# Optimization experiments

Hardware: AMD Instinct MI355X
Metric: run time of the kernel (lower is better)

The kernel has to match this reference:

```python
import jax, jax.numpy as jnp
import numpy as np

WIN = 7
HEADS = 6
DIM = 192

def _relative_position_index(ws):
    coords = np.stack(np.meshgrid(np.arange(ws[0]), np.arange(ws[1]), indexing='ij'))  # (2, Wh, Ww)
    flat = coords.reshape(2, -1)  # (2, N)
    rel = flat[:, :, None] - flat[:, None, :]  # (2, N, N)
    rel = rel.transpose(1, 2, 0).copy()
    rel[:, :, 0] += ws[0] - 1
    rel[:, :, 1] += ws[1] - 1
    idx = rel[:, :, 0] * (2 * ws[1] - 1) + rel[:, :, 1]
    return idx.astype(np.int32)  # (N, N)

def setup_inputs() -> dict:
    key = jax.random.key(0)
    ks = jax.random.split(key, 6)
    B_, N, C = 4096, WIN * WIN, DIM
    x = jax.random.normal(ks[0], (B_, N, C), dtype=jnp.float32)
    qkv_w = jax.random.normal(ks[1], (3 * C, C), dtype=jnp.float32) * 0.02
    qkv_b = jax.random.normal(ks[2], (3 * C,), dtype=jnp.float32) * 0.02
    proj_w = jax.random.normal(ks[3], (C, C), dtype=jnp.float32) * 0.02
    proj_b = jax.random.normal(ks[4], (C,), dtype=jnp.float32) * 0.02
    bias_table = jax.random.normal(ks[5], ((2 * WIN - 1) ** 2, HEADS), dtype=jnp.float32) * 0.02
    rel_idx = jnp.asarray(_relative_position_index((WIN, WIN)))  # (N, N) int32
    return {"x": x, "qkv_w": qkv_w, "qkv_b": qkv_b, "proj_w": proj_w,
            "proj_b": proj_b, "bias_table": bias_table, "rel_idx": rel_idx}

def reference(x, qkv_w, qkv_b, proj_w, proj_b, bias_table, rel_idx):
    B_, N, C = x.shape
    H = HEADS
    Dh = C // H
    scale = Dh ** -0.5
    # qkv: (B_, N, 3C) -> (3, B_, H, N, Dh)
    qkv = (x @ qkv_w.T + qkv_b).reshape(B_, N, 3, H, Dh).transpose(2, 0, 3, 1, 4)
    q, k, v = qkv[0], qkv[1], qkv[2]
    attn = jnp.einsum('bhnd,bhmd->bhnm', q, k) * scale  # (B_, H, N, N)
    bias = bias_table[rel_idx]  # (N, N, H)
    attn = attn + bias.transpose(2, 0, 1)[None]  # (1, H, N, N) broadcast
    attn = jax.nn.softmax(attn, axis=-1)
    out = jnp.einsum('bhnm,bhmd->bhnd', attn, v)  # (B_, H, N, Dh)
    out = out.transpose(0, 2, 1, 3).reshape(B_, N, C)
    return out @ proj_w.T + proj_b
```

## Files before the change

### kernel.cpp

```cpp
#include <hip/hip_runtime.h>
#include <hip/hip_bf16.h>

#define NTOK 49
#define HEADS 6
#define DIM 192
#define DH 32

typedef short s8v __attribute__((ext_vector_type(8)));
typedef float f4v __attribute__((ext_vector_type(4)));

#define MFMA16(a, b, c) __builtin_amdgcn_mfma_f32_16x16x32_bf16((a), (b), (c), 0, 0, 0)

__device__ inline short f2bf(float f) {
    __hip_bfloat16 h = __float2bfloat16(f);
    return __builtin_bit_cast(short, h);
}

__device__ inline s8v ld_bf8(const float* __restrict__ p) {
    float4 f0 = *(const float4*)p;
    float4 f1 = *(const float4*)(p + 4);
    s8v r;
    r[0] = f2bf(f0.x); r[1] = f2bf(f0.y); r[2] = f2bf(f0.z); r[3] = f2bf(f0.w);
    r[4] = f2bf(f1.x); r[5] = f2bf(f1.y); r[6] = f2bf(f1.z); r[7] = f2bf(f1.w);
    return r;
}

__global__ void prep_kernel(const float* __restrict__ qkv_w,
                            const float* __restrict__ proj_w,
                            const float* __restrict__ bias_table,
                            const int* __restrict__ rel_idx,
                            short* __restrict__ wq, short* __restrict__ wp,
                            float* __restrict__ biasM) {
    int tid = blockIdx.x * blockDim.x + threadIdx.x;
    int stride = gridDim.x * blockDim.x;
    for (int i = tid; i < 3 * DIM * DIM; i += stride) wq[i] = f2bf(qkv_w[i]);
    for (int i = tid; i < DIM * DIM; i += stride)     wp[i] = f2bf(proj_w[i]);
    for (int i = tid; i < HEADS * NTOK * NTOK; i += stride) {
        int h = i / (NTOK * NTOK), rc = i - h * (NTOK * NTOK);
        biasM[i] = bias_table[rel_idx[rc] * HEADS + h];
    }
}

__global__ __launch_bounds__(512) void qkv_kernel(
    const float* __restrict__ x, const short* __restrict__ wq,
    const float* __restrict__ qkv_b,
    short* __restrict__ q_ws, short* __restrict__ k_ws, short* __restrict__ v_ws)
{
    __shared__ __align__(16) short xs[64 * 200];
    __shared__ __align__(16) short vbuf[192 * 72];

    const int tid = threadIdx.x, w = tid >> 6, lane = tid & 63;
    const int quad = lane >> 4, l16 = lane & 15, b = blockIdx.x;

    {
        const float4* src = (const float4*)(x + (size_t)b * NTOK * DIM);
        for (int idx = tid; idx < 2352; idx += 512) {
            int n = idx / 48, c = idx % 48;
            float4 f = src[idx];
            short* dst = &xs[n * 200 + c * 4];
            dst[0] = f2bf(f.x); dst[1] = f2bf(f.y);
            dst[2] = f2bf(f.z); dst[3] = f2bf(f.w);
        }
        int* xz = (int*)xs;
        for (int i = tid; i < 1500; i += 512) xz[4900 + i] = 0;
        for (int i = tid; i < 192 * 23; i += 512) {
            int row = i / 23, t = 49 + i % 23;
            vbuf[row * 72 + t] = 0;
        }
    }
    __syncthreads();

    for (int nt = w; nt < 36; nt += 8) {
        const short* wrow = wq + (nt * 16 + l16) * DIM + quad * 8;
        s8v bw[6];
#pragma unroll
        for (int kb = 0; kb < 6; ++kb)
            bw[kb] = *(const s8v*)(wrow + kb * 32);

        f4v acc[4];
#pragma unroll
        for (int mt = 0; mt < 4; ++mt) acc[mt] = (f4v){0.f, 0.f, 0.f, 0.f};

#pragma unroll
        for (int kb = 0; kb < 6; ++kb) {
#pragma unroll
            for (int mt = 0; mt < 4; ++mt) {
                s8v a = *(const s8v*)&xs[(mt * 16 + l16) * 200 + kb * 32 + quad * 8];
                acc[mt] = MFMA16(a, bw[kb], acc[mt]);
            }
        }

        int t = nt / 12, hh = (nt % 12) >> 1, dh16 = (nt & 1) * 16;
        float bias = qkv_b[nt * 16 + l16];
        if (t == 2) {
            short* dst = &vbuf[(hh * DH + dh16 + l16) * 72];
#pragma unroll
            for (int mt = 0; mt < 4; ++mt)
#pragma unroll
                for (int r = 0; r < 4; ++r) {
                    int row = mt * 16 + quad * 4 + r;
                    if (row < NTOK) dst[row] = f2bf(acc[mt][r] + bias);
                }
        } else {
            float scale = (t == 0) ? 0.17677669529663689f : 1.0f;
            short* dst = (t == 0 ? q_ws : k_ws)
                       + (size_t)(b * HEADS + hh) * NTOK * DH + dh16 + l16;
#pragma unroll
            for (int mt = 0; mt < 4; ++mt)
#pragma unroll
                for (int r = 0; r < 4; ++r) {
                    int row = mt * 16 + quad * 4 + r;
                    if (row < NTOK) dst[row * DH] = f2bf((acc[mt][r] + bias) * scale);
                }
        }
    }
    __syncthreads();

    {
        short* dstbase = v_ws + (size_t)b * 192 * 64;
        for (int c = tid; c < 1536; c += 512) {
            int row = c >> 3, tk = (c & 7) * 8;
            *(int4*)(dstbase + row * 64 + tk) = *(const int4*)&vbuf[row * 72 + tk];
        }
    }
}

__global__ __launch_bounds__(384) void attn_kernel(
    const short* __restrict__ k_ws, const short* __restrict__ v_ws,
    const float* __restrict__ biasM, short* qo_ws )
{
    __shared__ __align__(16) short ps[6 * 64 * 72];

    const int tid = threadIdx.x, w = tid >> 6, lane = tid & 63;
    const int quad = lane >> 4, l16 = lane & 15, b = blockIdx.x;
    const int h = w;
    short* psw = ps + w * 4608;

    const short* qb = qo_ws + (size_t)(b * HEADS + h) * NTOK * DH;
    const short* kb = k_ws  + (size_t)(b * HEADS + h) * NTOK * DH;
    const short* vb = v_ws  + (size_t)(b * HEADS + h) * DH * 64;

    s8v aq[4], bk[4];
    for (int i = 0; i < 4; ++i)
        aq[i] = *(const s8v*)(qb + (i * 16 + l16) * DH + quad * 8);
    for (int i = 0; i < 4; ++i)
        bk[i] = *(const s8v*)(kb + (i * 16 + l16) * DH + quad * 8);

    f4v sacc[4][4];
    for (int mt = 0; mt < 4; ++mt)
        for (int nt = 0; nt < 4; ++nt)
            sacc[mt][nt] = MFMA16(aq[mt], bk[nt], ((f4v){0.f, 0.f, 0.f, 0.f}));

    const float* bmh = biasM + h * (NTOK * NTOK);
    for (int mt = 0; mt < 4; ++mt)
        for (int r = 0; r < 4; ++r) {
            int row = mt * 16 + quad * 4 + r;
            float sv[4];
            for (int nt = 0; nt < 4; ++nt) {
                int col = nt * 16 + l16;
                float s = sacc[mt][nt][r];
                if (col < NTOK) {
                    if (row < NTOK) s += bmh[row * NTOK + col];
                } else s = -30000.f;
                sv[nt] = s;
            }
            float m = fmaxf(fmaxf(sv[0], sv[1]), fmaxf(sv[2], sv[3]));
            for (int d = 1; d < 16; d <<= 1) m = fmaxf(m, __shfl_xor(m, d));
            float p[4], sum = 0.f;
            for (int nt = 0; nt < 4; ++nt) {
                p[nt] = exp2f((sv[nt] - m) * 1.4426950408889634f);
                sum += p[nt];
            }
            for (int d = 1; d < 16; d <<= 1) sum += __shfl_xor(sum, d);
            float inv = 1.f / sum;
            for (int nt = 0; nt < 4; ++nt)
                psw[row * 72 + nt * 16 + l16] = f2bf(p[nt] * inv);
        }

    f4v oacc[4][2];
    for (int mt = 0; mt < 4; ++mt)
        for (int nv = 0; nv < 2; ++nv) oacc[mt][nv] = (f4v){0.f, 0.f, 0.f, 0.f};
    for (int ks = 0; ks < 2; ++ks) {
        s8v bv[2];
        for (int nv = 0; nv < 2; ++nv)
            bv[nv] = *(const s8v*)(vb + (nv * 16 + l16) * 64 + ks * 32 + quad * 8);
        for (int mt = 0; mt < 4; ++mt) {
            s8v ap = *(const s8v*)&psw[(mt * 16 + l16) * 72 + ks * 32 + quad * 8];
            for (int nv = 0; nv < 2; ++nv)
                oacc[mt][nv] = MFMA16(ap, bv[nv], oacc[mt][nv]);
        }
    }

    __syncthreads();

    for (int mt = 0; mt < 4; ++mt)
        for (int nv = 0; nv < 2; ++nv)
            for (int r = 0; r < 4; ++r) {
                int row = mt * 16 + quad * 4 + r;
                if (row < NTOK)
                    qo_ws[((size_t)(b * NTOK + row) * HEADS + h) * DH + nv * 16 + l16] =
                        f2bf(oacc[mt][nv][r]);
            }
}

__global__ __launch_bounds__(256) void proj_kernel(
    const short* __restrict__ o_ws, const short* __restrict__ wp,
    const float* __restrict__ proj_b, float* __restrict__ out)
{
    __shared__ __align__(16) short os[64 * 200];
    const int tid = threadIdx.x, w = tid >> 6, lane = tid & 63;
    const int quad = lane >> 4, l16 = lane & 15, b = blockIdx.x;

    {
        const short* src = o_ws + (size_t)b * NTOK * DIM;
        for (int c = tid; c < 1176; c += 256) {
            int n = c / 24, cc = (c % 24) * 8;
            *(int4*)&os[n * 200 + cc] = *(const int4*)(src + n * DIM + cc);
        }
        int* oz = (int*)os;
        for (int i = tid; i < 1500; i += 256) oz[4900 + i] = 0;
    }
    __syncthreads();

    for (int nt = w; nt < 12; nt += 4) {
        const short* wrow = wp + (nt * 16 + l16) * DIM + quad * 8;
        s8v bw[6];
#pragma unroll
        for (int kb = 0; kb < 6; ++kb)
            bw[kb] = *(const s8v*)(wrow + kb * 32);

        f4v acc[4];
#pragma unroll
        for (int mt = 0; mt < 4; ++mt) acc[mt] = (f4v){0.f, 0.f, 0.f, 0.f};

#pragma unroll
        for (int kb = 0; kb < 6; ++kb) {
#pragma unroll
            for (int mt = 0; mt < 4; ++mt) {
                s8v a = *(const s8v*)&os[(mt * 16 + l16) * 200 + kb * 32 + quad * 8];
                acc[mt] = MFMA16(a, bw[kb], acc[mt]);
            }
        }

        int j0 = nt * 16 + l16;
        float bias = proj_b[j0];
        float* dst = out + (size_t)b * NTOK * DIM + j0;
#pragma unroll
        for (int mt = 0; mt < 4; ++mt)
#pragma unroll
            for (int r = 0; r < 4; ++r) {
                int row = mt * 16 + quad * 4 + r;
                if (row < NTOK) dst[row * DIM] = acc[mt][r] + bias;
            }
    }
}

__global__ __launch_bounds__(512) void winattn_fused(
    const float* __restrict__ x, const float* __restrict__ qkv_w,
    const float* __restrict__ qkv_b, const float* __restrict__ proj_w,
    const float* __restrict__ proj_b, const float* __restrict__ bias_table,
    const int* __restrict__ rel_idx, float* __restrict__ out)
{
    __shared__ __align__(16) short xs[64 * 200];
    __shared__ __align__(16) short qs[64 * 40];
    __shared__ __align__(16) short ks[64 * 40];
    __shared__ __align__(16) short vs[32 * 72];
    __shared__ __align__(16) short pp[64 * 72];

    const int tid = threadIdx.x, w = tid >> 6, lane = tid & 63;
    const int quad = lane >> 4, l16 = lane & 15, b = blockIdx.x;
    const int mt = w & 3, half = w >> 2;

    {
        const float4* src = (const float4*)(x + (size_t)b * NTOK * DIM);
        for (int idx = tid; idx < 2352; idx += 512) {
            int n = idx / 48, c = idx % 48;
            float4 f = src[idx];
            short* dst = &xs[n * 200 + c * 4];
            dst[0] = f2bf(f.x); dst[1] = f2bf(f.y);
            dst[2] = f2bf(f.z); dst[3] = f2bf(f.w);
        }
        int* xz = (int*)xs;
        for (int i = tid; i < 1500; i += 512) xz[4900 + i] = 0;
    }
    __syncthreads();

    f4v acc_p[6];
    for (int i = 0; i < 6; i++) acc_p[i] = (f4v){0.f, 0.f, 0.f, 0.f};

    for (int h = 0; h < HEADS; ++h) {
        {
            f4v acc[3];
            for (int i = 0; i < 3; i++) acc[i] = (f4v){0.f, 0.f, 0.f, 0.f};
            int jbase[3];
            for (int i = 0; i < 3; i++) {
                int tn = half * 3 + i;
                int t = tn >> 1, dpart = (tn & 1) * 16;
                jbase[i] = t * DIM + h * DH + dpart + l16;
            }
            for (int kb2 = 0; kb2 < 6; ++kb2) {
                s8v a = *(const s8v*)&xs[(mt * 16 + l16) * 200 + kb2 * 32 + quad * 8];
                for (int i = 0; i < 3; i++) {
                    s8v bf = ld_bf8(qkv_w + jbase[i] * DIM + kb2 * 32 + quad * 8);
                    acc[i] = MFMA16(a, bf, acc[i]);
                }
            }
            for (int i = 0; i < 3; i++) {
                int tn = half * 3 + i;
                int t = tn >> 1, dpart = (tn & 1) * 16;
                float bias = qkv_b[jbase[i]];
                for (int r = 0; r < 4; r++) {
                    int row = mt * 16 + quad * 4 + r;
                    float v = acc[i][r] + bias;
                    if (t == 0)      qs[row * 40 + dpart + l16] = f2bf(v * 0.17677669529663689f);
                    else if (t == 1) ks[row * 40 + dpart + l16] = f2bf(v);
                    else             vs[(dpart + l16) * 72 + row] = f2bf(v);
                }
            }
        }
        __syncthreads();
        if (w < 4) {
            f4v sacc[4];
            for (int i = 0; i < 4; i++) sacc[i] = (f4v){0.f, 0.f, 0.f, 0.f};
            s8v a = *(const s8v*)&qs[(w * 16 + l16) * 40 + quad * 8];
            for (int nt = 0; nt < 4; nt++) {
                s8v bf = *(const s8v*)&ks[(nt * 16 + l16) * 40 + quad * 8];
                sacc[nt] = MFMA16(a, bf, sacc[nt]);
            }
            for (int r = 0; r < 4; r++) {
                int row = w * 16 + quad * 4 + r;
                float sv[4];
                for (int nt = 0; nt < 4; nt++) {
                    int col = nt * 16 + l16;
                    float s = sacc[nt][r];
                    if (col < NTOK) {
                        if (row < NTOK)
                            s += bias_table[rel_idx[row * NTOK + col] * HEADS + h];
                    } else s = -30000.f;
                    sv[nt] = s;
                }
                float m = fmaxf(fmaxf(sv[0], sv[1]), fmaxf(sv[2], sv[3]));
                for (int d = 1; d < 16; d <<= 1) m = fmaxf(m, __shfl_xor(m, d));
                float p[4], sum = 0.f;
                for (int nt = 0; nt < 4; nt++) {
                    p[nt] = exp2f((sv[nt] - m) * 1.4426950408889634f);
                    sum += p[nt];
                }
                for (int d = 1; d < 16; d <<= 1) sum += __shfl_xor(sum, d);
                float inv = 1.f / sum;
                for (int nt = 0; nt < 4; nt++)
                    pp[row * 72 + nt * 16 + l16] = f2bf(p[nt] * inv);
            }
        }
        __syncthreads();
        {
            f4v oacc = (f4v){0.f, 0.f, 0.f, 0.f};
            for (int kb2 = 0; kb2 < 2; kb2++) {
                s8v a  = *(const s8v*)&pp[(mt * 16 + l16) * 72 + kb2 * 32 + quad * 8];
                s8v bf = *(const s8v*)&vs[(half * 16 + l16) * 72 + kb2 * 32 + quad * 8];
                oacc = MFMA16(a, bf, oacc);
            }
            for (int r = 0; r < 4; r++) {
                int row = mt * 16 + quad * 4 + r;
                qs[row * 40 + half * 16 + l16] = f2bf(oacc[r]);
            }
        }
        __syncthreads();
        {
            s8v a = *(const s8v*)&qs[(mt * 16 + l16) * 40 + quad * 8];
            for (int i = 0; i < 6; i++) {
                int ncol = half * 96 + i * 16 + l16;
                s8v bf = ld_bf8(proj_w + ncol * DIM + h * DH + quad * 8);
                acc_p[i] = MFMA16(a, bf, acc_p[i]);
            }
        }
        __syncthreads();
    }
    for (int i = 0; i < 6; i++) {
        int ncol = half * 96 + i * 16 + l16;
        float bias = proj_b[ncol];
        for (int r = 0; r < 4; r++) {
            int row = mt * 16 + quad * 4 + r;
            if (row < NTOK)
                out[((size_t)b * NTOK + row) * DIM + ncol] = acc_p[i][r] + bias;
        }
    }
}

extern "C" void kernel_launch(void* const* d_in, const int* in_sizes, int n_in,
                              void* d_out, int out_size, void* d_ws, size_t ws_size,
                              hipStream_t stream) {
    const float* x          = (const float*)d_in[0];
    const float* qkv_w      = (const float*)d_in[1];
    const float* qkv_b      = (const float*)d_in[2];
    const float* proj_w     = (const float*)d_in[3];
    const float* proj_b     = (const float*)d_in[4];
    const float* bias_table = (const float*)d_in[5];
    const int*   rel_idx    = (const int*)d_in[6];
    float*       out        = (float*)d_out;

    const int B_ = in_sizes[0] / (NTOK * DIM);

    const size_t sz_q  = (size_t)B_ * HEADS * NTOK * DH * 2;
    const size_t sz_k  = sz_q;
    const size_t sz_v  = (size_t)B_ * HEADS * DH * 64 * 2;
    const size_t sz_wq = (size_t)3 * DIM * DIM * 2;
    const size_t sz_wp = (size_t)DIM * DIM * 2;
    const size_t sz_bm = (size_t)HEADS * NTOK * NTOK * 4;
    const size_t need  = sz_q + sz_k + sz_v + sz_wq + sz_wp + sz_bm;

    if (ws_size >= need) {
        char* p = (char*)d_ws;
        short* q_ws  = (short*)p;                 p += sz_q;
        short* k_ws  = (short*)p;                 p += sz_k;
        short* v_ws  = (short*)p;                 p += sz_v;
        short* wq    = (short*)p;                 p += sz_wq;
        short* wp    = (short*)p;                 p += sz_wp;
        float* biasM = (float*)p;

        prep_kernel<<<dim3(128), dim3(256), 0, stream>>>(
            qkv_w, proj_w, bias_table, rel_idx, wq, wp, biasM);
        qkv_kernel<<<dim3(B_), dim3(512), 0, stream>>>(
            x, wq, qkv_b, q_ws, k_ws, v_ws);
        attn_kernel<<<dim3(B_), dim3(384), 0, stream>>>(
            k_ws, v_ws, biasM, q_ws);
        proj_kernel<<<dim3(B_), dim3(256), 0, stream>>>(
            q_ws, wp, proj_b, out);
    } else {
        winattn_fused<<<dim3(B_), dim3(512), 0, stream>>>(
            x, qkv_w, qkv_b, proj_w, proj_b, bias_table, rel_idx, out);
    }
}
```

Before: 653.0 us.

## Fuse QKV, attention and projection into one LDS-resident kernel per window

Adds a fused3 kernel that computes QKV, the windowed attention for all six heads and the output projection inside one block, holding q/k/v, probabilities and the attention output in about 156 KB of dynamic shared memory. This removes the global-memory round trips for the q/k/v and attention-output intermediates and two kernel launches. The trade-off is very high LDS use per block, allowing only one block per CU, and only 6 of 8 waves working in the attention phase and 8 of 12 tiles in a wave pass during projection. The old split path remains as a fallback when the attribute call fails.

```diff
diff --git a/kernel.cpp b/kernel.cpp
--- a/kernel.cpp
+++ b/kernel.cpp
@@ -41,13 +41,18 @@
     }
 }
 
-__global__ __launch_bounds__(512) void qkv_kernel(
+__global__ __launch_bounds__(512) void fused3(
     const float* __restrict__ x, const short* __restrict__ wq,
-    const float* __restrict__ qkv_b,
-    short* __restrict__ q_ws, short* __restrict__ k_ws, short* __restrict__ v_ws)
+    const float* __restrict__ qkv_b, const short* __restrict__ wp,
+    const float* __restrict__ proj_b, const float* __restrict__ biasM,
+    float* __restrict__ out)
 {
-    __shared__ __align__(16) short xs[64 * 200];
-    __shared__ __align__(16) short vbuf[192 * 72];
+    extern __shared__ __align__(16) short smem[];
+    short* xs = smem;
+    short* qs = smem + 12800;
+    short* ks = smem + 25600;
+    short* vs = smem + 38400;
+    short* ps = smem + 52224;
 
     const int tid = threadIdx.x, w = tid >> 6, lane = tid & 63;
     const int quad = lane >> 4, l16 = lane & 15, b = blockIdx.x;
@@ -63,6 +68,191 @@
         }
         int* xz = (int*)xs;
         for (int i = tid; i < 1500; i += 512) xz[4900 + i] = 0;
+    }
+    __syncthreads();
+
+    for (int nt = w; nt < 36; nt += 8) {
+        const short* wrow = wq + (nt * 16 + l16) * DIM + quad * 8;
+        s8v bw[6];
+#pragma unroll
+        for (int kb = 0; kb < 6; ++kb)
+            bw[kb] = *(const s8v*)(wrow + kb * 32);
+
+        f4v acc[4];
+#pragma unroll
+        for (int mt = 0; mt < 4; ++mt) acc[mt] = (f4v){0.f, 0.f, 0.f, 0.f};
+
+#pragma unroll
+        for (int kb = 0; kb < 6; ++kb) {
+#pragma unroll
+            for (int mt = 0; mt < 4; ++mt) {
+                s8v a = *(const s8v*)&xs[(mt * 16 + l16) * 200 + kb * 32 + quad * 8];
+                acc[mt] = MFMA16(a, bw[kb], acc[mt]);
+            }
+        }
+
+        int t = nt / 12, hh = (nt % 12) >> 1, dh16 = (nt & 1) * 16;
+        float bias = qkv_b[nt * 16 + l16];
+        if (t == 2) {
+            short* dst = &vs[(hh * DH + dh16 + l16) * 72];
+#pragma unroll
+            for (int mt = 0; mt < 4; ++mt)
+#pragma unroll
+                for (int r = 0; r < 4; ++r) {
+                    int row = mt * 16 + quad * 4 + r;
+                    dst[row] = f2bf(acc[mt][r] + bias);
+                }
+        } else {
+            float scale = (t == 0) ? 0.17677669529663689f : 1.0f;
+            short* dst = (t == 0 ? qs : ks) + hh * DH + dh16 + l16;
+#pragma unroll
+            for (int mt = 0; mt < 4; ++mt)
+#pragma unroll
+                for (int r = 0; r < 4; ++r) {
+                    int row = mt * 16 + quad * 4 + r;
+                    dst[row * 200] = f2bf((acc[mt][r] + bias) * scale);
+                }
+        }
+    }
+    __syncthreads();
+
+    if (w < HEADS) {
+        const int h = w;
+        short* psw = ps + w * 4608;
+
+        s8v aq[4], bk[4];
+#pragma unroll
+        for (int i = 0; i < 4; ++i)
+            aq[i] = *(const s8v*)&qs[(i * 16 + l16) * 200 + h * DH + quad * 8];
+#pragma unroll
+        for (int i = 0; i < 4; ++i)
+            bk[i] = *(const s8v*)&ks[(i * 16 + l16) * 200 + h * DH + quad * 8];
+
+        f4v sacc[4][4];
+#pragma unroll
+        for (int mt = 0; mt < 4; ++mt)
+#pragma unroll
+            for (int nt = 0; nt < 4; ++nt)
+                sacc[mt][nt] = MFMA16(aq[mt], bk[nt], ((f4v){0.f, 0.f, 0.f, 0.f}));
+
+        const float* bmh = biasM + h * (NTOK * NTOK);
+#pragma unroll
+        for (int mt = 0; mt < 4; ++mt)
+            for (int r = 0; r < 4; ++r) {
+                int row = mt * 16 + quad * 4 + r;
+                float sv[4];
+#pragma unroll
+                for (int nt = 0; nt < 4; ++nt) {
+                    int col = nt * 16 + l16;
+                    float s = sacc[mt][nt][r];
+                    if (col < NTOK) {
+                        if (row < NTOK) s += bmh[row * NTOK + col];
+                    } else s = -30000.f;
+                    sv[nt] = s;
+                }
+                float m = fmaxf(fmaxf(sv[0], sv[1]), fmaxf(sv[2], sv[3]));
+                for (int d = 1; d < 16; d <<= 1) m = fmaxf(m, __shfl_xor(m, d));
+                float p[4], sum = 0.f;
+#pragma unroll
+                for (int nt = 0; nt < 4; ++nt) {
+                    p[nt] = exp2f((sv[nt] - m) * 1.4426950408889634f);
+                    sum += p[nt];
+                }
+                for (int d = 1; d < 16; d <<= 1) sum += __shfl_xor(sum, d);
+                float inv = 1.f / sum;
+#pragma unroll
+                for (int nt = 0; nt < 4; ++nt)
+                    psw[row * 72 + nt * 16 + l16] = f2bf(p[nt] * inv);
+            }
+
+        f4v oacc[4][2];
+#pragma unroll
+        for (int mt = 0; mt < 4; ++mt)
+#pragma unroll
+            for (int nv = 0; nv < 2; ++nv) oacc[mt][nv] = (f4v){0.f, 0.f, 0.f, 0.f};
+#pragma unroll
+        for (int ks2 = 0; ks2 < 2; ++ks2) {
+            s8v bv[2];
+#pragma unroll
+            for (int nv = 0; nv < 2; ++nv)
+                bv[nv] = *(const s8v*)&vs[(h * DH + nv * 16 + l16) * 72 + ks2 * 32 + quad * 8];
+#pragma unroll
+            for (int mt = 0; mt < 4; ++mt) {
+                s8v ap = *(const s8v*)&psw[(mt * 16 + l16) * 72 + ks2 * 32 + quad * 8];
+#pragma unroll
+                for (int nv = 0; nv < 2; ++nv)
+                    oacc[mt][nv] = MFMA16(ap, bv[nv], oacc[mt][nv]);
+            }
+        }
+
+        short* os = xs;
+#pragma unroll
+        for (int mt = 0; mt < 4; ++mt)
+#pragma unroll
+            for (int nv = 0; nv < 2; ++nv)
+#pragma unroll
+                for (int r = 0; r < 4; ++r) {
+                    int row = mt * 16 + quad * 4 + r;
+                    os[row * 200 + h * DH + nv * 16 + l16] = f2bf(oacc[mt][nv][r]);
+                }
+    }
+    __syncthreads();
+
+    for (int nt = w; nt < 12; nt += 8) {
+        const short* wrow = wp + (nt * 16 + l16) * DIM + quad * 8;
+        s8v bw[6];
+#pragma unroll
+        for (int kb = 0; kb < 6; ++kb)
+            bw[kb] = *(const s8v*)(wrow + kb * 32);
+
+        f4v acc[4];
+#pragma unroll
+        for (int mt = 0; mt < 4; ++mt) acc[mt] = (f4v){0.f, 0.f, 0.f, 0.f};
+
+#pragma unroll
+        for (int kb = 0; kb < 6; ++kb) {
+#pragma unroll
+            for (int mt = 0; mt < 4; ++mt) {
+                s8v a = *(const s8v*)&xs[(mt * 16 + l16) * 200 + kb * 32 + quad * 8];
+                acc[mt] = MFMA16(a, bw[kb], acc[mt]);
+            }
+        }
+
+        int j0 = nt * 16 + l16;
+        float bias = proj_b[j0];
+        float* dst = out + (size_t)b * NTOK * DIM + j0;
+#pragma unroll
+        for (int mt = 0; mt < 4; ++mt)
+#pragma unroll
+            for (int r = 0; r < 4; ++r) {
+                int row = mt * 16 + quad * 4 + r;
+                if (row < NTOK) dst[row * DIM] = acc[mt][r] + bias;
+            }
+    }
+}
+
+__global__ __launch_bounds__(512) void qkv_kernel(
+    const float* __restrict__ x, const short* __restrict__ wq,
+    const float* __restrict__ qkv_b,
+    short* __restrict__ q_ws, short* __restrict__ k_ws, short* __restrict__ v_ws)
+{
+    __shared__ __align__(16) short xs[64 * 200];
+    __shared__ __align__(16) short vbuf[192 * 72];
+
+    const int tid = threadIdx.x, w = tid >> 6, lane = tid & 63;
+    const int quad = lane >> 4, l16 = lane & 15, b = blockIdx.x;
+
+    {
+        const float4* src = (const float4*)(x + (size_t)b * NTOK * DIM);
+        for (int idx = tid; idx < 2352; idx += 512) {
+            int n = idx / 48, c = idx % 48;
+            float4 f = src[idx];
+            short* dst = &xs[n * 200 + c * 4];
+            dst[0] = f2bf(f.x); dst[1] = f2bf(f.y);
+            dst[2] = f2bf(f.z); dst[3] = f2bf(f.w);
+        }
+        int* xz = (int*)xs;
+        for (int i = tid; i < 1500; i += 512) xz[4900 + i] = 0;
         for (int i = tid; i < 192 * 23; i += 512) {
             int row = i / 23, t = 49 + i % 23;
             vbuf[row * 72 + t] = 0;
@@ -74,22 +264,17 @@
         const short* wrow = wq + (nt * 16 + l16) * DIM + quad * 8;
         s8v bw[6];
 #pragma unroll
+        for (int kb = 0; kb < 6; ++kb) bw[kb] = *(const s8v*)(wrow + kb * 32);
+        f4v acc[4];
+#pragma unroll
+        for (int mt = 0; mt < 4; ++mt) acc[mt] = (f4v){0.f, 0.f, 0.f, 0.f};
+#pragma unroll
         for (int kb = 0; kb < 6; ++kb)
-            bw[kb] = *(const s8v*)(wrow + kb * 32);
-
-        f4v acc[4];
-#pragma unroll
-        for (int mt = 0; mt < 4; ++mt) acc[mt] = (f4v){0.f, 0.f, 0.f, 0.f};
-
-#pragma unroll
-        for (int kb = 0; kb < 6; ++kb) {
 #pragma unroll
             for (int mt = 0; mt < 4; ++mt) {
                 s8v a = *(const s8v*)&xs[(mt * 16 + l16) * 200 + kb * 32 + quad * 8];
                 acc[mt] = MFMA16(a, bw[kb], acc[mt]);
             }
-        }
-
         int t = nt / 12, hh = (nt % 12) >> 1, dh16 = (nt & 1) * 16;
         float bias = qkv_b[nt * 16 + l16];
         if (t == 2) {
@@ -127,7 +312,7 @@
 
 __global__ __launch_bounds__(384) void attn_kernel(
     const short* __restrict__ k_ws, const short* __restrict__ v_ws,
-    const float* __restrict__ biasM, short* qo_ws )
+    const float* __restrict__ biasM, short* qo_ws)
 {
     __shared__ __align__(16) short ps[6 * 64 * 72];
 
@@ -226,22 +411,17 @@
         const short* wrow = wp + (nt * 16 + l16) * DIM + quad * 8;
         s8v bw[6];
 #pragma unroll
+        for (int kb = 0; kb < 6; ++kb) bw[kb] = *(const s8v*)(wrow + kb * 32);
+        f4v acc[4];
+#pragma unroll
+        for (int mt = 0; mt < 4; ++mt) acc[mt] = (f4v){0.f, 0.f, 0.f, 0.f};
+#pragma unroll
         for (int kb = 0; kb < 6; ++kb)
-            bw[kb] = *(const s8v*)(wrow + kb * 32);
-
-        f4v acc[4];
-#pragma unroll
-        for (int mt = 0; mt < 4; ++mt) acc[mt] = (f4v){0.f, 0.f, 0.f, 0.f};
-
-#pragma unroll
-        for (int kb = 0; kb < 6; ++kb) {
 #pragma unroll
             for (int mt = 0; mt < 4; ++mt) {
                 s8v a = *(const s8v*)&os[(mt * 16 + l16) * 200 + kb * 32 + quad * 8];
                 acc[mt] = MFMA16(a, bw[kb], acc[mt]);
             }
-        }
-
         int j0 = nt * 16 + l16;
         float bias = proj_b[j0];
         float* dst = out + (size_t)b * NTOK * DIM + j0;
@@ -401,21 +581,41 @@
 
     const int B_ = in_sizes[0] / (NTOK * DIM);
 
+    const size_t FUSED_LDS = 159744;
+    static int smem_ok = -1;
+    if (smem_ok < 0) {
+        smem_ok = (hipFuncSetAttribute((const void*)fused3,
+                       hipFuncAttributeMaxDynamicSharedMemorySize,
+                       (int)FUSED_LDS) == hipSuccess) ? 1 : 0;
+    }
+
+    const size_t sz_wq = (size_t)3 * DIM * DIM * 2;
+    const size_t sz_wp = (size_t)DIM * DIM * 2;
+    const size_t sz_bm = (size_t)HEADS * NTOK * NTOK * 4;
+    const size_t need_fused = sz_wq + sz_wp + sz_bm;
+
     const size_t sz_q  = (size_t)B_ * HEADS * NTOK * DH * 2;
     const size_t sz_k  = sz_q;
     const size_t sz_v  = (size_t)B_ * HEADS * DH * 64 * 2;
-    const size_t sz_wq = (size_t)3 * DIM * DIM * 2;
-    const size_t sz_wp = (size_t)DIM * DIM * 2;
-    const size_t sz_bm = (size_t)HEADS * NTOK * NTOK * 4;
-    const size_t need  = sz_q + sz_k + sz_v + sz_wq + sz_wp + sz_bm;
-
-    if (ws_size >= need) {
+    const size_t need_split = sz_q + sz_k + sz_v + sz_wq + sz_wp + sz_bm;
+
+    if (smem_ok == 1 && ws_size >= need_fused) {
         char* p = (char*)d_ws;
-        short* q_ws  = (short*)p;                 p += sz_q;
-        short* k_ws  = (short*)p;                 p += sz_k;
-        short* v_ws  = (short*)p;                 p += sz_v;
-        short* wq    = (short*)p;                 p += sz_wq;
-        short* wp    = (short*)p;                 p += sz_wp;
+        short* wq    = (short*)p;  p += sz_wq;
+        short* wp    = (short*)p;  p += sz_wp;
+        float* biasM = (float*)p;
+
+        prep_kernel<<<dim3(128), dim3(256), 0, stream>>>(
+            qkv_w, proj_w, bias_table, rel_idx, wq, wp, biasM);
+        fused3<<<dim3(B_), dim3(512), FUSED_LDS, stream>>>(
+            x, wq, qkv_b, wp, proj_b, biasM, out);
+    } else if (ws_size >= need_split) {
+        char* p = (char*)d_ws;
+        short* q_ws  = (short*)p;  p += sz_q;
+        short* k_ws  = (short*)p;  p += sz_k;
+        short* v_ws  = (short*)p;  p += sz_v;
+        short* wq    = (short*)p;  p += sz_wq;
+        short* wp    = (short*)p;  p += sz_wp;
         float* biasM = (float*)p;
 
         prep_kernel<<<dim3(128), dim3(256), 0, stream>>>(
```

After: 575.1 us. 11.9% less time.
